# Kernel tuning notes

Measured on AMD Instinct MI355X. Metric: run time of the kernel, lower is better.

## Reference

```python
import jax, jax.numpy as jnp
import numpy as np

B, M, K = 8, 2048, 64          # clouds, points per cloud, max neighbors
C_IN, C_OUT, R = 64, 64, 0.2   # channels, radius
BN_EPS = 1e-5                  # BatchNorm eval: running_mean=0, running_var=1


def _bn(y, g, b):
    # eval-mode BatchNorm1d with running stats (0, 1)
    return g * y * (1.0 / jnp.sqrt(1.0 + BN_EPS)) + b


def _lin_init(key, fan_in, shape):
    s = 1.0 / np.sqrt(fan_in)
    return jax.random.uniform(key, shape, jnp.float32, -s, s)


def setup_inputs() -> dict:
    key = jax.random.key(0)
    ks = jax.random.split(key, 16)
    N = B * M
    pos = jax.random.uniform(ks[0], (N, 3), jnp.float32)
    x = jax.random.normal(ks[1], (N, C_IN), jnp.float32)
    nrm = jax.random.normal(ks[2], (N, 3), jnp.float32)
    normal = nrm / jnp.linalg.norm(nrm, axis=-1, keepdims=True)
    batch = jnp.repeat(jnp.arange(B, dtype=jnp.int32), M)
    return {
        "x": x, "pos": pos, "normal": normal, "batch": batch,
        # PointTransformerConv linear layers (value / key / query)
        "lin_w": _lin_init(ks[3], C_IN, (C_IN, C_OUT)),
        "lin_b": _lin_init(ks[4], C_IN, (C_OUT,)),
        "lin_src_w": _lin_init(ks[5], C_IN, (C_IN, C_OUT)),
        "lin_src_b": _lin_init(ks[6], C_IN, (C_OUT,)),
        "lin_dst_w": _lin_init(ks[7], C_IN, (C_IN, C_OUT)),
        "lin_dst_b": _lin_init(ks[8], C_IN, (C_OUT,)),
        # pos_nn = MLP([6, C_OUT]): Linear -> BN -> ReLU (Dropout off in eval)
        "pos_w": _lin_init(ks[9], 6, (6, C_OUT)),
        "pos_b": _lin_init(ks[10], 6, (C_OUT,)),
        "pos_g": jnp.ones((C_OUT,), jnp.float32),
        "pos_bt": jnp.zeros((C_OUT,), jnp.float32),
        # attn_nn = MLP([C_OUT, C_OUT])
        "attn_w": _lin_init(ks[11], C_OUT, (C_OUT, C_OUT)),
        "attn_b": _lin_init(ks[12], C_OUT, (C_OUT,)),
        "attn_g": jnp.ones((C_OUT,), jnp.float32),
        "attn_bt": jnp.zeros((C_OUT,), jnp.float32),
    }


def _forward(x, pos, normal, lin_w, lin_b, lin_src_w, lin_src_b,
             lin_dst_w, lin_dst_b, pos_w, pos_b, pos_g, pos_bt,
             attn_w, attn_b, attn_g, attn_bt):
    xb = x.reshape(B, M, C_IN)
    pb = pos.reshape(B, M, 3)
    nb = normal.reshape(B, M, 3)

    # radius(pos, pos, r, batch, batch, max_num_neighbors=K):
    # per-cloud pairwise sq-distances -> K nearest, masked to d <= r.
    d2 = jnp.sum((pb[:, :, None, :] - pb[:, None, :, :]) ** 2, axis=-1)  # [B,M,M]
    neg_d2, idx = jax.lax.top_k(-d2, K)                                   # [B,M,K]
    mask = (-neg_d2) <= R * R                                             # self always valid

    gather = jax.vmap(lambda a, i: a[i])  # per-cloud gather: [M,C],[M,K] -> [M,K,C]

    v = xb @ lin_w + lin_b          # value   [B,M,C]
    kf = xb @ lin_src_w + lin_src_b # key     [B,M,C]
    q = xb @ lin_dst_w + lin_dst_b  # query   [B,M,C]

    vj = gather(v, idx)             # [B,M,K,C]
    kj = gather(kf, idx)
    pj = gather(pb, idx)            # [B,M,K,3]
    nj = gather(nb, idx)

    rel = jnp.concatenate([pb[:, :, None, :] - pj,
                           nb[:, :, None, :] - nj], axis=-1)  # [B,M,K,6]
    delta = jax.nn.relu(_bn(rel @ pos_w + pos_b, pos_g, pos_bt))  # [B,M,K,C]

    alpha = jax.nn.relu(_bn((q[:, :, None, :] - kj + delta) @ attn_w + attn_b,
                            attn_g, attn_bt))                     # [B,M,K,C]
    alpha = jnp.where(mask[..., None], alpha, -jnp.inf)
    w = jax.nn.softmax(alpha, axis=2)                              # softmax over neighbors

    out = jnp.sum(w * (vj + delta), axis=2)                        # [B,M,C]
    return out.reshape(B * M, C_OUT)


def reference(x, pos, normal, batch, lin_w, lin_b, lin_src_w, lin_src_b,
              lin_dst_w, lin_dst_b, pos_w, pos_b, pos_g, pos_bt,
              attn_w, attn_b, attn_g, attn_bt):
    del batch  # batch ids are block-contiguous: encoded by the [B,M] reshape
    return _forward(x, pos, normal, lin_w, lin_b, lin_src_w, lin_src_b,
                    lin_dst_w, lin_dst_b, pos_w, pos_b, pos_g, pos_bt,
                    attn_w, attn_b, attn_g, attn_bt)
```

## Files before the change

kernel.cpp:

```cpp
#include <hip/hip_runtime.h>
#include <math.h>

#define BB 8
#define MM 2048
#define NTOT (BB*MM)
#define R2 0.04f
#define CAP 256

typedef _Float16 h8 __attribute__((ext_vector_type(8)));
typedef _Float16 h4 __attribute__((ext_vector_type(4)));
typedef float f32x4 __attribute__((ext_vector_type(4)));

__device__ __forceinline__ int swz(int row, int col) {
  return (row << 6) + ((((col >> 3) ^ (row & 7)) << 3) | (col & 7));
}

__device__ __forceinline__ unsigned long long shfl_xor_u64(unsigned long long x, int off) {
  int lo = __shfl_xor((int)(unsigned)(x & 0xFFFFFFFFull), off, 64);
  int hi = __shfl_xor((int)(unsigned)(x >> 32), off, 64);
  return (((unsigned long long)(unsigned)hi) << 32) | (unsigned)lo;
}
__device__ __forceinline__ unsigned long long wave_min_u64(unsigned long long x) {
#pragma unroll
  for (int off = 32; off; off >>= 1) {
    unsigned long long o = shfl_xor_u64(x, off);
    x = (o < x) ? o : x;
  }
  return x;
}
__device__ __forceinline__ unsigned long long wave_max_u64(unsigned long long x) {
#pragma unroll
  for (int off = 32; off; off >>= 1) {
    unsigned long long o = shfl_xor_u64(x, off);
    x = (o > x) ? o : x;
  }
  return x;
}

__global__ __launch_bounds__(256) void prep_w(
    const float* __restrict__ attn_w, const float* __restrict__ pos_w,
    const float* __restrict__ lin_w, const float* __restrict__ lsw, const float* __restrict__ ldw,
    const float* __restrict__ lsb, const float* __restrict__ ldb,
    const float* __restrict__ pos_b, const float* __restrict__ pos_g, const float* __restrict__ pos_bt,
    const float* __restrict__ attn_b, const float* __restrict__ attn_g, const float* __restrict__ attn_bt,
    unsigned short* __restrict__ w_img, unsigned short* __restrict__ pw_img,
    unsigned short* __restrict__ pj_img, float* __restrict__ bnc) {
  __shared__ float sWa[4096];
  __shared__ float sK[256], sQ[256];
  const int tid = threadIdx.x, blk = blockIdx.x;
  for (int i = tid; i < 4096; i += 256) sWa[i] = attn_w[i];
  {
    const int r = tid >> 6, c = tid & 63;
    sK[tid] = lsw[(blk * 4 + r) * 64 + c];
    sQ[tid] = ldw[(blk * 4 + r) * 64 + c];
  }
  __syncthreads();
  const int idx = blk * 256 + tid;
  const int d = idx >> 6, cc = idx & 63;
  const int lr = tid >> 6;
  float wka_v = 0.f, wqa_v = 0.f;
  for (int m = 0; m < 64; ++m) {
    const float wac = sWa[m * 64 + cc];
    wka_v = fmaf(sK[lr * 64 + m], wac, wka_v);
    wqa_v = fmaf(sQ[lr * 64 + m], wac, wqa_v);
  }
  const int sp = swz(cc, d);
  w_img[sp] = __builtin_bit_cast(unsigned short, (_Float16)sWa[d * 64 + cc]);
  const float v0 = lin_w[idx];
  const _Float16 h0 = (_Float16)v0;
  pj_img[sp] = __builtin_bit_cast(unsigned short, h0);
  pj_img[4096 + sp] = __builtin_bit_cast(unsigned short, (_Float16)(v0 - (float)h0));
  const _Float16 h1 = (_Float16)wka_v;
  pj_img[8192 + sp] = __builtin_bit_cast(unsigned short, h1);
  pj_img[12288 + sp] = __builtin_bit_cast(unsigned short, (_Float16)(wka_v - (float)h1));
  const _Float16 h2 = (_Float16)wqa_v;
  pj_img[16384 + sp] = __builtin_bit_cast(unsigned short, h2);
  pj_img[20480 + sp] = __builtin_bit_cast(unsigned short, (_Float16)(wqa_v - (float)h2));
  if (idx < 64 * 24) {
    const int col = idx / 24, k = idx - col * 24;
    const float v = (k < 6) ? pos_w[k * 64 + col] : 0.f;
    pw_img[idx] = __builtin_bit_cast(unsigned short, (_Float16)v);
  }
  if (blk == 0 && tid < 64) {
    float bk = 0.f, bq = 0.f;
    for (int m = 0; m < 64; ++m) {
      const float wac = sWa[m * 64 + tid];
      bk = fmaf(lsb[m], wac, bk);
      bq = fmaf(ldb[m], wac, bq);
    }
    const float bninv = 1.0f / sqrtf(1.0f + 1e-5f);
    const float pA = pos_g[tid] * bninv;
    bnc[tid] = pA;
    bnc[64 + tid] = pA * pos_b[tid] + pos_bt[tid];
    const float aA = attn_g[tid] * bninv;
    bnc[128 + tid] = aA;
    bnc[192 + tid] = aA * (attn_b[tid] + bq - bk) + attn_bt[tid];
  }
}

__global__ __launch_bounds__(256, 2) void proj_mfma(
    const float* __restrict__ x, const unsigned short* __restrict__ pj_img,
    const float* __restrict__ b0,
    float* __restrict__ kv2, float* __restrict__ qwr) {
  __shared__ __align__(16) unsigned short s_xh[4096];
  __shared__ __align__(16) unsigned short s_xl[4096];
  __shared__ __align__(16) unsigned short s_w6[6 * 4096];
  const int tid = threadIdx.x;
  const int r0 = blockIdx.x << 6;
  for (int i = tid; i < 3072; i += 256)
    ((uint4*)s_w6)[i] = ((const uint4*)pj_img)[i];
  {
    const int row = tid >> 2, seg = tid & 3;
    const float* xr = x + (((size_t)(r0 + row)) << 6) + (seg << 4);
    float xb[16];
#pragma unroll
    for (int q = 0; q < 4; ++q) *(float4*)&xb[q * 4] = ((const float4*)xr)[q];
    h8 c0h, c1h, c0l, c1l;
#pragma unroll
    for (int e = 0; e < 8; ++e) {
      const _Float16 h0 = (_Float16)xb[e];
      c0h[e] = h0; c0l[e] = (_Float16)(xb[e] - (float)h0);
      const _Float16 h1 = (_Float16)xb[e + 8];
      c1h[e] = h1; c1l[e] = (_Float16)(xb[e + 8] - (float)h1);
    }
    const int base = row << 6;
    const int oi0 = base + ((((seg << 1) | 0) ^ (row & 7)) << 3);
    const int oi1 = base + ((((seg << 1) | 1) ^ (row & 7)) << 3);
    *(h8*)&s_xh[oi0] = c0h; *(h8*)&s_xh[oi1] = c1h;
    *(h8*)&s_xl[oi0] = c0l; *(h8*)&s_xl[oi1] = c1l;
  }
  __syncthreads();
  const int wv = tid >> 6, lane = tid & 63, lrow = lane >> 4, lcol = lane & 15;
  const int col = (wv << 4) + lcol;
  f32x4 acc[3][4];
#pragma unroll
  for (int o = 0; o < 3; ++o)
#pragma unroll
    for (int mt = 0; mt < 4; ++mt) acc[o][mt] = (f32x4){0.f, 0.f, 0.f, 0.f};
#pragma unroll
  for (int ks = 0; ks < 2; ++ks) {
    const int kc = lrow + (ks << 2);
    const int boff = (col << 6) + ((kc ^ (col & 7)) << 3);
    const h8 bh0 = *(const h8*)&s_w6[boff];
    const h8 bl0 = *(const h8*)&s_w6[4096 + boff];
    const h8 bh1 = *(const h8*)&s_w6[8192 + boff];
    const h8 bl1 = *(const h8*)&s_w6[12288 + boff];
    const h8 bh2 = *(const h8*)&s_w6[16384 + boff];
    const h8 bl2 = *(const h8*)&s_w6[20480 + boff];
#pragma unroll
    for (int mt = 0; mt < 4; ++mt) {
      const int m = (mt << 4) + lcol;
      const int aoff = (m << 6) + ((kc ^ (m & 7)) << 3);
      const h8 ah = *(const h8*)&s_xh[aoff];
      const h8 al = *(const h8*)&s_xl[aoff];
      acc[0][mt] = __builtin_amdgcn_mfma_f32_16x16x32_f16(ah, bh0, acc[0][mt], 0, 0, 0);
      acc[0][mt] = __builtin_amdgcn_mfma_f32_16x16x32_f16(al, bh0, acc[0][mt], 0, 0, 0);
      acc[0][mt] = __builtin_amdgcn_mfma_f32_16x16x32_f16(ah, bl0, acc[0][mt], 0, 0, 0);
      acc[1][mt] = __builtin_amdgcn_mfma_f32_16x16x32_f16(ah, bh1, acc[1][mt], 0, 0, 0);
      acc[1][mt] = __builtin_amdgcn_mfma_f32_16x16x32_f16(al, bh1, acc[1][mt], 0, 0, 0);
      acc[1][mt] = __builtin_amdgcn_mfma_f32_16x16x32_f16(ah, bl1, acc[1][mt], 0, 0, 0);
      acc[2][mt] = __builtin_amdgcn_mfma_f32_16x16x32_f16(ah, bh2, acc[2][mt], 0, 0, 0);
      acc[2][mt] = __builtin_amdgcn_mfma_f32_16x16x32_f16(al, bh2, acc[2][mt], 0, 0, 0);
      acc[2][mt] = __builtin_amdgcn_mfma_f32_16x16x32_f16(ah, bl2, acc[2][mt], 0, 0, 0);
    }
  }
  const float bb0 = b0[col];
#pragma unroll
  for (int mt = 0; mt < 4; ++mt)
#pragma unroll
    for (int r = 0; r < 4; ++r) {
      const size_t row = (size_t)(r0 + (mt << 4) + (lrow << 2) + r);
      *(float2*)&kv2[(row << 7) + (col << 1)] =
          make_float2(acc[1][mt][r], acc[0][mt][r] + bb0);
      qwr[(row << 6) + col] = acc[2][mt][r];
    }
}

__global__ __launch_bounds__(256) void knn_kernel(const float* __restrict__ pos,
                                                  unsigned* __restrict__ nbr) {
  __shared__ float spos[MM * 3];
  __shared__ unsigned long long slist[4][CAP];
  const int bidx = blockIdx.x;
  const int b = bidx >> 9;
  const int qblk = bidx & 511;
  const int tid = threadIdx.x;
  const float* pc = pos + (size_t)b * MM * 3;
  for (int i = tid; i < MM * 3 / 4; i += 256)
    ((float4*)spos)[i] = ((const float4*)pc)[i];
  __syncthreads();
  const int wv = tid >> 6, lane = tid & 63;
  const int q = (qblk << 2) + wv;
  const float qx = spos[q * 3 + 0], qy = spos[q * 3 + 1], qz = spos[q * 3 + 2];
  unsigned bits[32];
  unsigned cnt = 0;
#pragma unroll
  for (int i = 0; i < 32; ++i) {
    const int j = lane + (i << 6);
    const float dx = qx - spos[j * 3 + 0];
    const float dy = qy - spos[j * 3 + 1];
    const float dz = qz - spos[j * 3 + 2];
    const float d2 = __fadd_rn(__fadd_rn(__fmul_rn(dx, dx), __fmul_rn(dy, dy)), __fmul_rn(dz, dz));
    const unsigned bt = __float_as_uint(d2);
    bits[i] = bt;
    const bool val = (d2 <= R2);
    const unsigned long long mb = __ballot(val);
    if (val) {
      const unsigned off = cnt + (unsigned)__popcll(mb & ((1ull << lane) - 1ull));
      if (off < CAP) slist[wv][off] = (((unsigned long long)bt) << 32) | (unsigned)j;
    }
    cnt += (unsigned)__popcll(mb);
  }
  __syncthreads();
  unsigned outv;
  if (cnt <= 64u) {
    if (lane < (int)cnt) outv = ((unsigned)slist[wv][lane]) | 0x80000000u;
    else                 outv = 0u;
  } else if (cnt <= (unsigned)CAP) {
    unsigned long long s0, s1, s2, s3, t;
    s0 = (lane       < (int)cnt) ? slist[wv][lane      ] : ~0ull;
    s1 = (lane + 64  < (int)cnt) ? slist[wv][lane + 64 ] : ~0ull;
    s2 = (lane + 128 < (int)cnt) ? slist[wv][lane + 128] : ~0ull;
    s3 = (lane + 192 < (int)cnt) ? slist[wv][lane + 192] : ~0ull;
    if (s1 < s0) { t = s0; s0 = s1; s1 = t; }
    if (s3 < s2) { t = s2; s2 = s3; s3 = t; }
    if (s2 < s0) { t = s0; s0 = s2; s2 = t; }
    if (s3 < s1) { t = s1; s1 = s3; s3 = t; }
    if (s2 < s1) { t = s1; s1 = s2; s2 = t; }
    if (cnt <= 128u) {
      const int pops = (int)cnt - 64;
      int rl = (cnt > (unsigned)lane) ? (int)((cnt - (unsigned)lane + 63u) >> 6) : 0;
      if (rl > 4) rl = 4;
      int ti = rl - 1;
      for (int p = 0; p < pops; ++p) {
        const unsigned long long mx =
            (ti == 3) ? s3 : (ti == 2) ? s2 : (ti == 1) ? s1 : (ti == 0) ? s0 : 0ull;
        const unsigned long long g = wave_max_u64(mx);
        if (ti >= 0 && mx == g) ti--;
      }
      const int c = ti + 1;
      const unsigned long long b0 = __ballot(c & 1);
      const unsigned long long b1 = __ballot(c & 2);
      const unsigned long long b2 = __ballot(c & 4);
      const unsigned long long lm = (1ull << lane) - 1ull;
      const int pre = __popcll(b0 & lm) + 2 * __popcll(b1 & lm) + 4 * __popcll(b2 & lm);
      if (c > 0) slist[wv][pre + 0] = s0;
      if (c > 1) slist[wv][pre + 1] = s1;
      if (c > 2) slist[wv][pre + 2] = s2;
      if (c > 3) slist[wv][pre + 3] = s3;
      __asm volatile("s_waitcnt lgkmcnt(0)" ::: "memory");
      outv = ((unsigned)slist[wv][lane]) | 0x80000000u;
    } else {
      unsigned long long my = 0;
      for (int it = 0; it < 64; ++it) {
        const unsigned long long gg = wave_min_u64(s0);
        if (lane == it) my = gg;
        if (s0 == gg) { s0 = s1; s1 = s2; s2 = s3; s3 = ~0ull; }
      }
      outv = ((unsigned)my) | 0x80000000u;
    }
  } else {
    unsigned long long cur = ~0ull;
#pragma unroll
    for (int i = 0; i < 32; ++i) {
      const unsigned long long k = (((unsigned long long)bits[i]) << 32) | (unsigned)(lane + (i << 6));
      cur = (k < cur) ? k : cur;
    }
    unsigned long long my = 0;
    for (int it = 0; it < 64; ++it) {
      const unsigned long long gg = wave_min_u64(cur);
      if (lane == it) my = gg;
      if (cur == gg) {
        cur = ~0ull;
#pragma unroll
        for (int i = 0; i < 32; ++i) {
          const unsigned long long k = (((unsigned long long)bits[i]) << 32) | (unsigned)(lane + (i << 6));
          if (k > gg && k < cur) cur = k;
        }
      }
    }
    const float d2s = __uint_as_float((unsigned)(my >> 32));
    outv = ((unsigned)my) | ((d2s <= R2) ? 0x80000000u : 0u);
  }
  nbr[((size_t)(b * MM + q)) * 64 + lane] = outv;
}

__global__ __launch_bounds__(256, 4) void ptc_kernel(
    const float* __restrict__ pos, const float* __restrict__ nrm,
    const float* __restrict__ kv2, const float* __restrict__ qwr,
    const unsigned* __restrict__ nbr,
    const unsigned short* __restrict__ w_img, const unsigned short* __restrict__ pw_img,
    const float* __restrict__ bnc,
    float* __restrict__ out) {
  __shared__ __align__(16) unsigned short s_t[4096];
  __shared__ __align__(16) unsigned short s_relh[64 * 16];
  const int qi = blockIdx.x;
  const int b = qi >> 11;
  const int tid = threadIdx.x;
  const int wv = tid >> 6, lane = tid & 63;
  const int lrow = lane >> 4, lcol = lane & 15;
  const int col = (wv << 4) + lcol;

  const h8 bh0 = *(const h8*)&w_img[(col << 6) + ((lrow ^ (col & 7)) << 3)];
  const h8 bh1 = *(const h8*)&w_img[(col << 6) + (((lrow + 4) ^ (col & 7)) << 3)];
  const h4 bpw = *(const h4*)&pw_img[col * 24 + (lrow << 2)];
  const float pA = bnc[col], pB = bnc[64 + col];
  const float aA = bnc[128 + col];
  const float qwc = qwr[(size_t)qi * 64 + col];
  const float aBq = fmaf(aA, qwc, bnc[192 + col]);

  uint4 sraw[4];
#pragma unroll
  for (int mt = 0; mt < 4; ++mt)
    sraw[mt] = *(const uint4*)&nbr[(size_t)qi * 64 + (mt << 4) + (lrow << 2)];
  float kwv[16], vvv[16];
  unsigned mbits = 0;
#pragma unroll
  for (int mt = 0; mt < 4; ++mt) {
    const unsigned sv[4] = {sraw[mt].x, sraw[mt].y, sraw[mt].z, sraw[mt].w};
#pragma unroll
    for (int r = 0; r < 4; ++r) {
      const int i = (mt << 2) + r;
      const unsigned s = sv[r];
      mbits |= ((s >> 31) & 1u) << i;
      const size_t jg = ((size_t)(b << 11) + (size_t)(s & 0x7FFFFFFFu));
      const float2 kv = *(const float2*)&kv2[(jg << 7) + (col << 1)];
      kwv[i] = kv.x;
      vvv[i] = kv.y;
    }
  }

  if (tid < 64) {
    const unsigned s = nbr[(size_t)qi * 64 + tid];
    const int jg = (b << 11) + (int)(s & 0x7FFFFFFFu);
    h8 hv;
    hv[0] = (_Float16)(pos[(size_t)qi * 3 + 0] - pos[(size_t)jg * 3 + 0]);
    hv[1] = (_Float16)(pos[(size_t)qi * 3 + 1] - pos[(size_t)jg * 3 + 1]);
    hv[2] = (_Float16)(pos[(size_t)qi * 3 + 2] - pos[(size_t)jg * 3 + 2]);
    hv[3] = (_Float16)(nrm[(size_t)qi * 3 + 0] - nrm[(size_t)jg * 3 + 0]);
    hv[4] = (_Float16)(nrm[(size_t)qi * 3 + 1] - nrm[(size_t)jg * 3 + 1]);
    hv[5] = (_Float16)(nrm[(size_t)qi * 3 + 2] - nrm[(size_t)jg * 3 + 2]);
    hv[6] = (_Float16)0.f; hv[7] = (_Float16)0.f;
    *(h8*)&s_relh[tid * 16] = hv;
    h8 zz = (h8)(_Float16)0.f;
    *(h8*)&s_relh[tid * 16 + 8] = zz;
  }
  __syncthreads();

  f32x4 dacc[4];
#pragma unroll
  for (int mt = 0; mt < 4; ++mt) {
    const h4 ar = *(const h4*)&s_relh[(((mt << 4) + lcol) << 4) + (lrow << 2)];
    dacc[mt] = __builtin_amdgcn_mfma_f32_16x16x16f16(ar, bpw, (f32x4){0.f, 0.f, 0.f, 0.f}, 0, 0, 0);
  }

  float def[16];
#pragma unroll
  for (int mt = 0; mt < 4; ++mt) {
#pragma unroll
    for (int r = 0; r < 4; ++r) {
      const int i = (mt << 2) + r;
      const int n = (mt << 4) + (lrow << 2) + r;
      const float de = fmaxf(fmaf(pA, dacc[mt][r], pB), 0.f);
      def[i] = de;
      *(_Float16*)&s_t[swz(n, col)] = (_Float16)de;
    }
  }
  __syncthreads();

  f32x4 acc[4];
#pragma unroll
  for (int mt = 0; mt < 4; ++mt) acc[mt] = (f32x4){0.f, 0.f, 0.f, 0.f};
#pragma unroll
  for (int mt = 0; mt < 4; ++mt) {
    const int m = (mt << 4) + lcol;
    const h8 ah0 = *(const h8*)&s_t[(m << 6) + ((lrow ^ (m & 7)) << 3)];
    acc[mt] = __builtin_amdgcn_mfma_f32_16x16x32_f16(ah0, bh0, acc[mt], 0, 0, 0);
    const h8 ah1 = *(const h8*)&s_t[(m << 6) + (((lrow + 4) ^ (m & 7)) << 3)];
    acc[mt] = __builtin_amdgcn_mfma_f32_16x16x32_f16(ah1, bh1, acc[mt], 0, 0, 0);
  }

  float ps = 0.f;
#pragma unroll
  for (int mt = 0; mt < 4; ++mt) {
#pragma unroll
    for (int r = 0; r < 4; ++r) {
      const int i = (mt << 2) + r;
      const float al = fmaxf(fmaf(aA, acc[mt][r] - kwv[i], aBq), 0.f);
      const float e = ((mbits >> i) & 1u) ? __expf(al) : 0.f;
      kwv[i] = e;
      ps += e;
    }
  }
  ps += __shfl_xor(ps, 16, 64);
  ps += __shfl_xor(ps, 32, 64);

  float o = 0.f;
#pragma unroll
  for (int i = 0; i < 16; ++i) o = fmaf(kwv[i], vvv[i] + def[i], o);
  o += __shfl_xor(o, 16, 64);
  o += __shfl_xor(o, 32, 64);
  if (lrow == 0) out[(size_t)qi * 64 + col] = o * (1.0f / ps);
}

extern "C" void kernel_launch(void* const* d_in, const int* in_sizes, int n_in,
                              void* d_out, int out_size, void* d_ws, size_t ws_size,
                              hipStream_t stream) {
  const float* x      = (const float*)d_in[0];
  const float* pos    = (const float*)d_in[1];
  const float* nrm    = (const float*)d_in[2];
  const float* lin_w  = (const float*)d_in[4];
  const float* lin_b  = (const float*)d_in[5];
  const float* lsw    = (const float*)d_in[6];
  const float* lsb    = (const float*)d_in[7];
  const float* ldw    = (const float*)d_in[8];
  const float* ldb    = (const float*)d_in[9];
  const float* pos_w  = (const float*)d_in[10];
  const float* pos_b  = (const float*)d_in[11];
  const float* pos_g  = (const float*)d_in[12];
  const float* pos_bt = (const float*)d_in[13];
  const float* attn_w = (const float*)d_in[14];
  const float* attn_b = (const float*)d_in[15];
  const float* attn_g = (const float*)d_in[16];
  const float* attn_bt= (const float*)d_in[17];
  float* out = (float*)d_out;

  float* wsf = (float*)d_ws;
  float* kv2  = wsf;
  float* qwr  = wsf + (size_t)NTOT * 128;
  unsigned* nbr = (unsigned*)(wsf + (size_t)NTOT * 192);
  unsigned short* w_img  = (unsigned short*)(wsf + (size_t)NTOT * 192 + (size_t)NTOT * 64);
  unsigned short* pw_img = w_img + 4096;
  unsigned short* pj_img = pw_img + 1536;
  float* bnc  = (float*)(pj_img + 24576);

  prep_w<<<16, 256, 0, stream>>>(attn_w, pos_w, lin_w, lsw, ldw, lsb, ldb,
                                 pos_b, pos_g, pos_bt, attn_b, attn_g, attn_bt,
                                 w_img, pw_img, pj_img, bnc);
  proj_mfma<<<NTOT / 64, 256, 0, stream>>>(x, pj_img, lin_b, kv2, qwr);
  knn_kernel<<<BB * (MM / 4), 256, 0, stream>>>(pos, nbr);
  ptc_kernel<<<NTOT, 256, 0, stream>>>(
      pos, nrm, kv2, qwr, nbr, w_img, pw_img, bnc, out);
}
```

Baseline: 129.7 us.

## Merge projection and kNN kernels into one launch, read weights from global

The projection GEMM and the radius-kNN search now run as two block ranges of a single kernel that shares one 32 KB LDS buffer, so one launch replaces two and the independent work can overlap on the GPU. The projection no longer stages its 48 KB weight image in LDS and reads B fragments directly from global memory, which cuts the LDS footprint so both roles fit the shared allocation. The ptc kernel's relative-position staging stride is padded from 16 to 24 halves to reduce LDS bank conflicts. The trade-offs are uncached global weight loads in the GEMM, and kNN blocks inheriting the launch bound of two blocks per CU.

```diff
diff --git a/kernel.cpp b/kernel.cpp
--- a/kernel.cpp
+++ b/kernel.cpp
@@ -98,17 +98,12 @@
   }
 }
 
-__global__ __launch_bounds__(256, 2) void proj_mfma(
+__device__ __forceinline__ void proj_body(
     const float* __restrict__ x, const unsigned short* __restrict__ pj_img,
-    const float* __restrict__ b0,
-    float* __restrict__ kv2, float* __restrict__ qwr) {
-  __shared__ __align__(16) unsigned short s_xh[4096];
-  __shared__ __align__(16) unsigned short s_xl[4096];
-  __shared__ __align__(16) unsigned short s_w6[6 * 4096];
+    const float* __restrict__ b0, float* __restrict__ kv2, float* __restrict__ qwr,
+    unsigned short* s_xh, unsigned short* s_xl, int bid) {
   const int tid = threadIdx.x;
-  const int r0 = blockIdx.x << 6;
-  for (int i = tid; i < 3072; i += 256)
-    ((uint4*)s_w6)[i] = ((const uint4*)pj_img)[i];
+  const int r0 = bid << 6;
   {
     const int row = tid >> 2, seg = tid & 3;
     const float* xr = x + (((size_t)(r0 + row)) << 6) + (seg << 4);
@@ -141,12 +136,12 @@
   for (int ks = 0; ks < 2; ++ks) {
     const int kc = lrow + (ks << 2);
     const int boff = (col << 6) + ((kc ^ (col & 7)) << 3);
-    const h8 bh0 = *(const h8*)&s_w6[boff];
-    const h8 bl0 = *(const h8*)&s_w6[4096 + boff];
-    const h8 bh1 = *(const h8*)&s_w6[8192 + boff];
-    const h8 bl1 = *(const h8*)&s_w6[12288 + boff];
-    const h8 bh2 = *(const h8*)&s_w6[16384 + boff];
-    const h8 bl2 = *(const h8*)&s_w6[20480 + boff];
+    const h8 bh0 = *(const h8*)&pj_img[boff];
+    const h8 bl0 = *(const h8*)&pj_img[4096 + boff];
+    const h8 bh1 = *(const h8*)&pj_img[8192 + boff];
+    const h8 bl1 = *(const h8*)&pj_img[12288 + boff];
+    const h8 bh2 = *(const h8*)&pj_img[16384 + boff];
+    const h8 bl2 = *(const h8*)&pj_img[20480 + boff];
 #pragma unroll
     for (int mt = 0; mt < 4; ++mt) {
       const int m = (mt << 4) + lcol;
@@ -176,19 +171,18 @@
     }
 }
 
-__global__ __launch_bounds__(256) void knn_kernel(const float* __restrict__ pos,
-                                                  unsigned* __restrict__ nbr) {
-  __shared__ float spos[MM * 3];
-  __shared__ unsigned long long slist[4][CAP];
-  const int bidx = blockIdx.x;
-  const int b = bidx >> 9;
-  const int qblk = bidx & 511;
+__device__ __forceinline__ void knn_body(
+    const float* __restrict__ pos, unsigned* __restrict__ nbr,
+    float* spos, unsigned long long* slistb, int bid) {
+  const int b = bid >> 9;
+  const int qblk = bid & 511;
   const int tid = threadIdx.x;
   const float* pc = pos + (size_t)b * MM * 3;
   for (int i = tid; i < MM * 3 / 4; i += 256)
     ((float4*)spos)[i] = ((const float4*)pc)[i];
   __syncthreads();
   const int wv = tid >> 6, lane = tid & 63;
+  unsigned long long* slist = slistb + wv * CAP;
   const int q = (qblk << 2) + wv;
   const float qx = spos[q * 3 + 0], qy = spos[q * 3 + 1], qz = spos[q * 3 + 2];
   unsigned bits[32];
@@ -206,21 +200,21 @@
     const unsigned long long mb = __ballot(val);
     if (val) {
       const unsigned off = cnt + (unsigned)__popcll(mb & ((1ull << lane) - 1ull));
-      if (off < CAP) slist[wv][off] = (((unsigned long long)bt) << 32) | (unsigned)j;
+      if (off < CAP) slist[off] = (((unsigned long long)bt) << 32) | (unsigned)j;
     }
     cnt += (unsigned)__popcll(mb);
   }
   __syncthreads();
   unsigned outv;
   if (cnt <= 64u) {
-    if (lane < (int)cnt) outv = ((unsigned)slist[wv][lane]) | 0x80000000u;
+    if (lane < (int)cnt) outv = ((unsigned)slist[lane]) | 0x80000000u;
     else                 outv = 0u;
   } else if (cnt <= (unsigned)CAP) {
     unsigned long long s0, s1, s2, s3, t;
-    s0 = (lane       < (int)cnt) ? slist[wv][lane      ] : ~0ull;
-    s1 = (lane + 64  < (int)cnt) ? slist[wv][lane + 64 ] : ~0ull;
-    s2 = (lane + 128 < (int)cnt) ? slist[wv][lane + 128] : ~0ull;
-    s3 = (lane + 192 < (int)cnt) ? slist[wv][lane + 192] : ~0ull;
+    s0 = (lane       < (int)cnt) ? slist[lane      ] : ~0ull;
+    s1 = (lane + 64  < (int)cnt) ? slist[lane + 64 ] : ~0ull;
+    s2 = (lane + 128 < (int)cnt) ? slist[lane + 128] : ~0ull;
+    s3 = (lane + 192 < (int)cnt) ? slist[lane + 192] : ~0ull;
     if (s1 < s0) { t = s0; s0 = s1; s1 = t; }
     if (s3 < s2) { t = s2; s2 = s3; s3 = t; }
     if (s2 < s0) { t = s0; s0 = s2; s2 = t; }
@@ -243,12 +237,12 @@
       const unsigned long long b2 = __ballot(c & 4);
       const unsigned long long lm = (1ull << lane) - 1ull;
       const int pre = __popcll(b0 & lm) + 2 * __popcll(b1 & lm) + 4 * __popcll(b2 & lm);
-      if (c > 0) slist[wv][pre + 0] = s0;
-      if (c > 1) slist[wv][pre + 1] = s1;
-      if (c > 2) slist[wv][pre + 2] = s2;
-      if (c > 3) slist[wv][pre + 3] = s3;
+      if (c > 0) slist[pre + 0] = s0;
+      if (c > 1) slist[pre + 1] = s1;
+      if (c > 2) slist[pre + 2] = s2;
+      if (c > 3) slist[pre + 3] = s3;
       __asm volatile("s_waitcnt lgkmcnt(0)" ::: "memory");
-      outv = ((unsigned)slist[wv][lane]) | 0x80000000u;
+      outv = ((unsigned)slist[lane]) | 0x80000000u;
     } else {
       unsigned long long my = 0;
       for (int it = 0; it < 64; ++it) {
@@ -284,6 +278,20 @@
   nbr[((size_t)(b * MM + q)) * 64 + lane] = outv;
 }
 
+__global__ __launch_bounds__(256, 2) void proj_knn(
+    const float* __restrict__ x, const unsigned short* __restrict__ pj_img,
+    const float* __restrict__ b0, float* __restrict__ kv2, float* __restrict__ qwr,
+    const float* __restrict__ pos, unsigned* __restrict__ nbr) {
+  __shared__ __align__(16) unsigned char smem[32768];
+  if (blockIdx.x < NTOT / 64) {
+    proj_body(x, pj_img, b0, kv2, qwr,
+              (unsigned short*)smem, (unsigned short*)(smem + 8192), blockIdx.x);
+  } else {
+    knn_body(pos, nbr, (float*)smem,
+             (unsigned long long*)(smem + 24576), blockIdx.x - NTOT / 64);
+  }
+}
+
 __global__ __launch_bounds__(256, 4) void ptc_kernel(
     const float* __restrict__ pos, const float* __restrict__ nrm,
     const float* __restrict__ kv2, const float* __restrict__ qwr,
@@ -292,7 +300,7 @@
     const float* __restrict__ bnc,
     float* __restrict__ out) {
   __shared__ __align__(16) unsigned short s_t[4096];
-  __shared__ __align__(16) unsigned short s_relh[64 * 16];
+  __shared__ __align__(16) unsigned short s_relh[64 * 24];
   const int qi = blockIdx.x;
   const int b = qi >> 11;
   const int tid = threadIdx.x;
@@ -340,16 +348,16 @@
     hv[4] = (_Float16)(nrm[(size_t)qi * 3 + 1] - nrm[(size_t)jg * 3 + 1]);
     hv[5] = (_Float16)(nrm[(size_t)qi * 3 + 2] - nrm[(size_t)jg * 3 + 2]);
     hv[6] = (_Float16)0.f; hv[7] = (_Float16)0.f;
-    *(h8*)&s_relh[tid * 16] = hv;
+    *(h8*)&s_relh[tid * 24] = hv;
     h8 zz = (h8)(_Float16)0.f;
-    *(h8*)&s_relh[tid * 16 + 8] = zz;
+    *(h8*)&s_relh[tid * 24 + 8] = zz;
   }
   __syncthreads();
 
   f32x4 dacc[4];
 #pragma unroll
   for (int mt = 0; mt < 4; ++mt) {
-    const h4 ar = *(const h4*)&s_relh[(((mt << 4) + lcol) << 4) + (lrow << 2)];
+    const h4 ar = *(const h4*)&s_relh[((mt << 4) + lcol) * 24 + (lrow << 2)];
     dacc[mt] = __builtin_amdgcn_mfma_f32_16x16x16f16(ar, bpw, (f32x4){0.f, 0.f, 0.f, 0.f}, 0, 0, 0);
   }
 
@@ -436,8 +444,8 @@
   prep_w<<<16, 256, 0, stream>>>(attn_w, pos_w, lin_w, lsw, ldw, lsb, ldb,
                                  pos_b, pos_g, pos_bt, attn_b, attn_g, attn_bt,
                                  w_img, pw_img, pj_img, bnc);
-  proj_mfma<<<NTOT / 64, 256, 0, stream>>>(x, pj_img, lin_b, kv2, qwr);
-  knn_kernel<<<BB * (MM / 4), 256, 0, stream>>>(pos, nbr);
+  proj_knn<<<NTOT / 64 + BB * (MM / 4), 256, 0, stream>>>(
+      x, pj_img, lin_b, kv2, qwr, pos, nbr);
   ptc_kernel<<<NTOT, 256, 0, stream>>>(
       pos, nrm, kv2, qwr, nbr, w_img, pw_img, bnc, out);
 }
```

Measured after the change: 122.1 us. -5.9%, faster.
